# Performance work log

Hardware: AMD Instinct MI355X
Metric: run time of the kernel (lower is better)

Reference implementation:

```python
import jax, jax.numpy as jnp
import numpy as np

N = 50000       # nodes
E = 800000      # edges (before self-loops)
NFEAT = 256
NHID = 64
NHEADS = 4
NOUT = 256
NEG_SLOPE = 0.2
BN_EPS = 1e-5
LN_EPS = 1e-5


def setup_inputs() -> dict:
    key = jax.random.key(0)
    ks = jax.random.split(key, 12)
    g = lambda k, s: (jax.random.normal(k, s, dtype=jnp.float32) * 0.05)
    inp = {
        "x": jax.random.normal(ks[0], (N, NFEAT), dtype=jnp.float32),
        "edge_index": jax.random.randint(ks[1], (2, E), 0, N, dtype=jnp.int32),
        # layer 1: GATConv(NFEAT, NHID, heads=NHEADS, concat=True)
        "W1": g(ks[2], (NFEAT, NHEADS * NHID)),
        "att_src1": g(ks[3], (NHEADS, NHID)),
        "att_dst1": g(ks[4], (NHEADS, NHID)),
        "bias1": jnp.zeros((NHEADS * NHID,), jnp.float32),
        # layer 2: GATConv(NHEADS*NHID, NOUT, heads=1, concat=False)
        "W2": g(ks[5], (NHEADS * NHID, NOUT)),
        "att_src2": g(ks[6], (1, NOUT)),
        "att_dst2": g(ks[7], (1, NOUT)),
        "bias2": jnp.zeros((NOUT,), jnp.float32),
        # BatchNorm1d (eval mode: running stats)
        "bn_gamma": jnp.ones((NOUT,), jnp.float32),
        "bn_beta": jnp.zeros((NOUT,), jnp.float32),
        "bn_mean": g(ks[8], (NOUT,)),
        "bn_var": jnp.ones((NOUT,), jnp.float32),
        # LayerNorm
        "ln_gamma": jnp.ones((NOUT,), jnp.float32),
        "ln_beta": jnp.zeros((NOUT,), jnp.float32),
    }
    return inp


def _gat_conv(x, edge_index, W, att_src, att_dst, bias, concat):
    """PyG-style GATConv (eval mode, add_self_loops=True)."""
    n = x.shape[0]
    H, C = att_src.shape
    xp = (x @ W).reshape(n, H, C)                    # [N,H,C]
    loop = jnp.arange(n, dtype=edge_index.dtype)
    src = jnp.concatenate([edge_index[0], loop])     # message source j
    dst = jnp.concatenate([edge_index[1], loop])     # aggregation target i
    a_src = jnp.einsum("nhc,hc->nh", xp, att_src)    # [N,H]
    a_dst = jnp.einsum("nhc,hc->nh", xp, att_dst)
    e = jax.nn.leaky_relu(a_src[src] + a_dst[dst], NEG_SLOPE)  # [Etot,H]
    # segment softmax over edges sharing the same dst
    m = jax.ops.segment_max(e, dst, num_segments=n)
    e = jnp.exp(e - m[dst])
    denom = jax.ops.segment_sum(e, dst, num_segments=n)
    alpha = e / (denom[dst] + 1e-16)                 # [Etot,H]
    out = jax.ops.segment_sum(alpha[:, :, None] * xp[src], dst, num_segments=n)  # [N,H,C]
    out = out.reshape(n, H * C) if concat else out.mean(axis=1)
    return out + bias


def reference(x, edge_index, W1, att_src1, att_dst1, bias1,
              W2, att_src2, att_dst2, bias2,
              bn_gamma, bn_beta, bn_mean, bn_var, ln_gamma, ln_beta):
    # eval mode: F.dropout is identity
    h = jax.nn.elu(_gat_conv(x, edge_index, W1, att_src1, att_dst1, bias1, True))
    h = jax.nn.elu(_gat_conv(h, edge_index, W2, att_src2, att_dst2, bias2, False))
    # BatchNorm1d (eval: running stats)
    h = (h - bn_mean) * jax.lax.rsqrt(bn_var + BN_EPS) * bn_gamma + bn_beta
    # LayerNorm over last dim
    mu = h.mean(axis=-1, keepdims=True)
    var = jnp.mean((h - mu) ** 2, axis=-1, keepdims=True)
    h = (h - mu) * jax.lax.rsqrt(var + LN_EPS) * ln_gamma + ln_beta
    return h
```

## Files before the change

### kernel.cpp

```cpp
#include <hip/hip_runtime.h>
#include <cstddef>
#include <cstdint>

#define NNODES 50000
#define NEDGES 800000
#define FDIM   256

#define SCAN_BLOCKS 256
#define SCAN_CHUNK  ((NNODES + SCAN_BLOCKS - 1) / SCAN_BLOCKS)

typedef __attribute__((ext_vector_type(8))) short short8;
typedef __attribute__((ext_vector_type(8))) unsigned short ushort8;
typedef __attribute__((ext_vector_type(4))) float f32x4;

__device__ __forceinline__ float leaky_exp(float a) {
    float e = a > 0.f ? a : 0.2f * a;
    return __expf(e);
}
__device__ __forceinline__ unsigned short f2bf(float f) {
    uint32_t u = __builtin_bit_cast(uint32_t, f);
    u += 0x7fffu + ((u >> 16) & 1u);
    return (unsigned short)(u >> 16);
}
__device__ __forceinline__ float bf2f(unsigned short h) {
    uint32_t u = ((uint32_t)h) << 16;
    return __builtin_bit_cast(float, u);
}
__device__ __forceinline__ float bflo(uint32_t u) {
    return __builtin_bit_cast(float, u << 16);
}
__device__ __forceinline__ float bfhi(uint32_t u) {
    return __builtin_bit_cast(float, u & 0xffff0000u);
}
__device__ __forceinline__ float rlanef(float v, int l) {
    return __builtin_bit_cast(float,
        __builtin_amdgcn_readlane(__builtin_bit_cast(int, v), l));
}

__global__ __launch_bounds__(256) void cvt_k(const float* __restrict__ in,
                                             unsigned short* __restrict__ out,
                                             int n8) {
    int i = blockIdx.x * 256 + threadIdx.x;
    if (i >= n8) return;
    const float4* p = (const float4*)in + (size_t)i * 2;
    float4 a = p[0], b = p[1];
    ushort8 r;
    r[0] = f2bf(a.x); r[1] = f2bf(a.y); r[2] = f2bf(a.z); r[3] = f2bf(a.w);
    r[4] = f2bf(b.x); r[5] = f2bf(b.y); r[6] = f2bf(b.z); r[7] = f2bf(b.w);
    *(ushort8*)(out + (size_t)i * 8) = r;
}

__global__ __launch_bounds__(256) void wprep_k(const float* __restrict__ W,
                                               unsigned short* __restrict__ Wt) {
    int n = blockIdx.x, k = threadIdx.x;
    Wt[n * 256 + k] = f2bf(W[k * 256 + n]);
}

__global__ __launch_bounds__(256) void gemm_mfma(const unsigned short* __restrict__ A,
                                                 const unsigned short* __restrict__ Bt,
                                                 unsigned short* __restrict__ C, int M) {
    __shared__ unsigned short As[128 * 64];
    __shared__ unsigned short Bs[128 * 64];
    const int t = threadIdx.x;
    const int lane = t & 63, wid = t >> 6;
    const int wr = wid >> 1, wc = wid & 1;
    const int bm = blockIdx.x * 128;
    const int bn = blockIdx.y * 128;
    f32x4 acc[4][4] = {};
    const int lrow = t >> 3, lslot = t & 7;
    for (int k0 = 0; k0 < 256; k0 += 64) {
        __syncthreads();
#pragma unroll
        for (int i = 0; i < 4; ++i) {
            int row = lrow + 32 * i;
            int ga = bm + row; ga = ga < M ? ga : M - 1;
            uint4 av = *(const uint4*)(A + (size_t)ga * FDIM + k0 + lslot * 8);
            *(uint4*)(As + row * 64 + ((lslot ^ (row & 7)) << 3)) = av;
            uint4 bv = *(const uint4*)(Bt + (size_t)(bn + row) * FDIM + k0 + lslot * 8);
            *(uint4*)(Bs + row * 64 + ((lslot ^ (row & 7)) << 3)) = bv;
        }
        __syncthreads();
#pragma unroll
        for (int ks = 0; ks < 2; ++ks) {
            const int kq = ks * 4 + (lane >> 4);
            short8 a[4], b[4];
#pragma unroll
            for (int f = 0; f < 4; ++f) {
                int ra = wr * 64 + f * 16 + (lane & 15);
                a[f] = *(const short8*)(As + ra * 64 + ((kq ^ (ra & 7)) << 3));
                int rb = wc * 64 + f * 16 + (lane & 15);
                b[f] = *(const short8*)(Bs + rb * 64 + ((kq ^ (rb & 7)) << 3));
            }
#pragma unroll
            for (int mf = 0; mf < 4; ++mf)
#pragma unroll
                for (int nf = 0; nf < 4; ++nf)
                    acc[mf][nf] = __builtin_amdgcn_mfma_f32_16x16x32_bf16(
                        a[mf], b[nf], acc[mf][nf], 0, 0, 0);
        }
    }
    const int col0 = bn + wc * 64 + (lane & 15);
    const int row00 = bm + wr * 64 + (lane >> 4) * 4;
#pragma unroll
    for (int mf = 0; mf < 4; ++mf)
#pragma unroll
        for (int nf = 0; nf < 4; ++nf) {
            f32x4 v = acc[mf][nf];
            int col = col0 + nf * 16;
#pragma unroll
            for (int r = 0; r < 4; ++r) {
                int row = row00 + mf * 16 + r;
                if (row < M) C[(size_t)row * FDIM + col] = f2bf(v[r]);
            }
        }
}

template <int H>
__global__ __launch_bounds__(256) void aprep_k(const unsigned short* __restrict__ xp,
                                               const float* __restrict__ atts,
                                               const float* __restrict__ attd,
                                               float* __restrict__ as_,
                                               float* __restrict__ ad_) {
    const int lane = threadIdx.x & 63;
    const int n = blockIdx.x * 4 + (threadIdx.x >> 6);
    if (n >= NNODES) return;
    const int c = lane << 2;
    ushort4 u = *(const ushort4*)(xp + (size_t)n * FDIM + c);
    float v0 = bf2f(u.x), v1 = bf2f(u.y), v2 = bf2f(u.z), v3 = bf2f(u.w);
    float4 s4 = *(const float4*)(atts + c);
    float4 d4 = *(const float4*)(attd + c);
    float ss = v0 * s4.x + v1 * s4.y + v2 * s4.z + v3 * s4.w;
    float sd = v0 * d4.x + v1 * d4.y + v2 * d4.z + v3 * d4.w;
    constexpr int G = 64 / H;
#pragma unroll
    for (int off = 1; off < G; off <<= 1) {
        ss += __shfl_xor(ss, off);
        sd += __shfl_xor(sd, off);
    }
    if ((lane & (G - 1)) == 0) {
        int h = lane / G;
        as_[n * H + h] = ss;
        ad_[n * H + h] = sd;
    }
}

__global__ __launch_bounds__(256) void hist_k(const int* __restrict__ ei,
                                              int* __restrict__ deg) {
    int e = blockIdx.x * 256 + threadIdx.x;
    if (e < NEDGES) atomicAdd(&deg[ei[NEDGES + e]], 1);
}

__global__ __launch_bounds__(256) void scanA_k(const int* __restrict__ deg,
                                               int* __restrict__ bsum) {
    const int b = blockIdx.x, t = threadIdx.x;
    const int i = b * SCAN_CHUNK + t;
    int v = (t < SCAN_CHUNK && i < NNODES) ? deg[i] : 0;
#pragma unroll
    for (int off = 1; off < 64; off <<= 1) v += __shfl_xor(v, off);
    __shared__ int ws[4];
    if ((t & 63) == 0) ws[t >> 6] = v;
    __syncthreads();
    if (t == 0) bsum[b] = ws[0] + ws[1] + ws[2] + ws[3];
}

__global__ __launch_bounds__(256) void scanB_k(const int* __restrict__ bsum,
                                               int* __restrict__ boff,
                                               int* __restrict__ rowptr) {
    const int t = threadIdx.x;
    const int lane = t & 63, wid = t >> 6;
    int orig = bsum[t];
    int v = orig;
#pragma unroll
    for (int off = 1; off < 64; off <<= 1) {
        int u = __shfl_up(v, off);
        if (lane >= off) v += u;
    }
    __shared__ int ws[4], wo[4];
    if (lane == 63) ws[wid] = v;
    __syncthreads();
    if (t == 0) {
        int a = 0;
        for (int k = 0; k < 4; ++k) { wo[k] = a; a += ws[k]; }
        rowptr[NNODES] = a;
    }
    __syncthreads();
    boff[t] = wo[wid] + v - orig;
}

__global__ __launch_bounds__(256) void scanC_k(const int* __restrict__ deg,
                                               const int* __restrict__ boff,
                                               int* __restrict__ rowptr) {
    const int b = blockIdx.x, t = threadIdx.x;
    const int i = b * SCAN_CHUNK + t;
    const bool ok = (t < SCAN_CHUNK && i < NNODES);
    int orig = ok ? deg[i] : 0;
    int v = orig;
    const int lane = t & 63, wid = t >> 6;
#pragma unroll
    for (int off = 1; off < 64; off <<= 1) {
        int u = __shfl_up(v, off);
        if (lane >= off) v += u;
    }
    __shared__ int ws[4], wo[4];
    if (lane == 63) ws[wid] = v;
    __syncthreads();
    if (t == 0) {
        int a = 0;
        for (int k = 0; k < 4; ++k) { wo[k] = a; a += ws[k]; }
    }
    __syncthreads();
    if (ok) rowptr[i] = boff[b] + wo[wid] + v - orig;
}

__global__ __launch_bounds__(256) void scatter_k(const int* __restrict__ ei,
                                                 const int* __restrict__ rowptr,
                                                 int* __restrict__ deg,
                                                 int* __restrict__ ssrc) {
    int e = blockIdx.x * 256 + threadIdx.x;
    if (e >= NEDGES) return;
    int s = ei[e], d = ei[NEDGES + e];
    int old = atomicSub(&deg[d], 1);
    ssrc[rowptr[d + 1] - old] = s;
}

__global__ __launch_bounds__(256) void gather1_k(const unsigned short* __restrict__ xp,
                                                 const float* __restrict__ as_,
                                                 const float* __restrict__ ad_,
                                                 const int* __restrict__ rowptr,
                                                 const int* __restrict__ ssrc,
                                                 const float* __restrict__ bias,
                                                 unsigned short* __restrict__ out) {
    const int lane = threadIdx.x & 63;
    const int n = blockIdx.x * 4 + (threadIdx.x >> 6);
    if (n >= NNODES) return;
    const int h = lane >> 4;
    const int c = lane << 2;
    const int eloc = lane >> 2;
    const int hh = lane & 3;
    const float adW = ad_[n * 4 + hh];
    float a0 = 0.f, a1 = 0.f, a2 = 0.f, a3 = 0.f, den = 0.f;
    const int beg = rowptr[n], end = rowptr[n + 1];
    for (int base = beg; base < end; base += 16) {
        int my_e = base + eloc;
        float wv = 0.f; int sv = 0;
        if (my_e < end) {
            sv = ssrc[my_e];
            wv = leaky_exp(as_[sv * 4 + hh] + adW);
        }
        const int cnt = min(16, end - base);
        int e = 0;
        for (; e + 4 <= cnt; e += 4) {
            int s0 = __builtin_amdgcn_readlane(sv, (e + 0) << 2);
            int s1 = __builtin_amdgcn_readlane(sv, (e + 1) << 2);
            int s2 = __builtin_amdgcn_readlane(sv, (e + 2) << 2);
            int s3 = __builtin_amdgcn_readlane(sv, (e + 3) << 2);
            uint2 u0 = *(const uint2*)(xp + (((unsigned)s0 << 8) + (unsigned)c));
            uint2 u1 = *(const uint2*)(xp + (((unsigned)s1 << 8) + (unsigned)c));
            uint2 u2 = *(const uint2*)(xp + (((unsigned)s2 << 8) + (unsigned)c));
            uint2 u3 = *(const uint2*)(xp + (((unsigned)s3 << 8) + (unsigned)c));
            float w0 = __shfl(wv, ((e + 0) << 2) | h);
            float w1 = __shfl(wv, ((e + 1) << 2) | h);
            float w2 = __shfl(wv, ((e + 2) << 2) | h);
            float w3 = __shfl(wv, ((e + 3) << 2) | h);
            a0 += w0 * bflo(u0.x) + w1 * bflo(u1.x) + w2 * bflo(u2.x) + w3 * bflo(u3.x);
            a1 += w0 * bfhi(u0.x) + w1 * bfhi(u1.x) + w2 * bfhi(u2.x) + w3 * bfhi(u3.x);
            a2 += w0 * bflo(u0.y) + w1 * bflo(u1.y) + w2 * bflo(u2.y) + w3 * bflo(u3.y);
            a3 += w0 * bfhi(u0.y) + w1 * bfhi(u1.y) + w2 * bfhi(u2.y) + w3 * bfhi(u3.y);
            den += (w0 + w1) + (w2 + w3);
        }
        for (; e < cnt; ++e) {
            int s0 = __builtin_amdgcn_readlane(sv, e << 2);
            uint2 u0 = *(const uint2*)(xp + (((unsigned)s0 << 8) + (unsigned)c));
            float w0 = __shfl(wv, (e << 2) | h);
            a0 += w0 * bflo(u0.x); a1 += w0 * bfhi(u0.x);
            a2 += w0 * bflo(u0.y); a3 += w0 * bfhi(u0.y);
            den += w0;
        }
    }
    {
        float w = leaky_exp(as_[n * 4 + h] + ad_[n * 4 + h]);
        uint2 u = *(const uint2*)(xp + (((unsigned)n << 8) + (unsigned)c));
        a0 += w * bflo(u.x); a1 += w * bfhi(u.x);
        a2 += w * bflo(u.y); a3 += w * bfhi(u.y);
        den += w;
    }
    const float inv = 1.f / (den + 1e-16f);
    float4 b4 = *(const float4*)(bias + c);
    float o[4] = {a0 * inv + b4.x, a1 * inv + b4.y,
                  a2 * inv + b4.z, a3 * inv + b4.w};
#pragma unroll
    for (int j = 0; j < 4; ++j) o[j] = o[j] > 0.f ? o[j] : __expf(o[j]) - 1.f;
    ushort4 r;
    r.x = f2bf(o[0]); r.y = f2bf(o[1]); r.z = f2bf(o[2]); r.w = f2bf(o[3]);
    *(ushort4*)(out + (size_t)n * FDIM + c) = r;
}

__global__ __launch_bounds__(256) void gather2_k(const unsigned short* __restrict__ xp,
                                                 const float* __restrict__ as_,
                                                 const float* __restrict__ ad_,
                                                 const int* __restrict__ rowptr,
                                                 const int* __restrict__ ssrc,
                                                 const float* __restrict__ bias,
                                                 const float* __restrict__ bng,
                                                 const float* __restrict__ bnb,
                                                 const float* __restrict__ bnm,
                                                 const float* __restrict__ bnv,
                                                 const float* __restrict__ lng,
                                                 const float* __restrict__ lnb,
                                                 float* __restrict__ out) {
    const int lane = threadIdx.x & 63;
    const int n = blockIdx.x * 4 + (threadIdx.x >> 6);
    if (n >= NNODES) return;
    const int c = lane << 2;
    const float adn = ad_[n];
    float a0 = 0.f, a1 = 0.f, a2 = 0.f, a3 = 0.f, den = 0.f;
    const int beg = rowptr[n], end = rowptr[n + 1];
    for (int base = beg; base < end; base += 64) {
        int my_e = base + lane;
        float wv = 0.f; int sv = 0;
        if (my_e < end) {
            sv = ssrc[my_e];
            wv = leaky_exp(as_[sv] + adn);
        }
        const int cnt = min(64, end - base);
        int e = 0;
        for (; e + 4 <= cnt; e += 4) {
            int s0 = __builtin_amdgcn_readlane(sv, e + 0);
            int s1 = __builtin_amdgcn_readlane(sv, e + 1);
            int s2 = __builtin_amdgcn_readlane(sv, e + 2);
            int s3 = __builtin_amdgcn_readlane(sv, e + 3);
            uint2 u0 = *(const uint2*)(xp + (((unsigned)s0 << 8) + (unsigned)c));
            uint2 u1 = *(const uint2*)(xp + (((unsigned)s1 << 8) + (unsigned)c));
            uint2 u2 = *(const uint2*)(xp + (((unsigned)s2 << 8) + (unsigned)c));
            uint2 u3 = *(const uint2*)(xp + (((unsigned)s3 << 8) + (unsigned)c));
            float w0 = rlanef(wv, e + 0);
            float w1 = rlanef(wv, e + 1);
            float w2 = rlanef(wv, e + 2);
            float w3 = rlanef(wv, e + 3);
            a0 += w0 * bflo(u0.x) + w1 * bflo(u1.x) + w2 * bflo(u2.x) + w3 * bflo(u3.x);
            a1 += w0 * bfhi(u0.x) + w1 * bfhi(u1.x) + w2 * bfhi(u2.x) + w3 * bfhi(u3.x);
            a2 += w0 * bflo(u0.y) + w1 * bflo(u1.y) + w2 * bflo(u2.y) + w3 * bflo(u3.y);
            a3 += w0 * bfhi(u0.y) + w1 * bfhi(u1.y) + w2 * bfhi(u2.y) + w3 * bfhi(u3.y);
            den += (w0 + w1) + (w2 + w3);
        }
        for (; e < cnt; ++e) {
            int s0 = __builtin_amdgcn_readlane(sv, e);
            uint2 u0 = *(const uint2*)(xp + (((unsigned)s0 << 8) + (unsigned)c));
            float w0 = rlanef(wv, e);
            a0 += w0 * bflo(u0.x); a1 += w0 * bfhi(u0.x);
            a2 += w0 * bflo(u0.y); a3 += w0 * bfhi(u0.y);
            den += w0;
        }
    }
    {
        float w = leaky_exp(as_[n] + adn);
        uint2 u = *(const uint2*)(xp + (((unsigned)n << 8) + (unsigned)c));
        a0 += w * bflo(u.x); a1 += w * bfhi(u.x);
        a2 += w * bflo(u.y); a3 += w * bfhi(u.y);
        den += w;
    }
    const float inv = 1.f / (den + 1e-16f);
    float vals[4] = {a0 * inv, a1 * inv, a2 * inv, a3 * inv};
#pragma unroll
    for (int j = 0; j < 4; ++j) {
        float o = vals[j] + bias[c + j];
        o = o > 0.f ? o : __expf(o) - 1.f;
        o = (o - bnm[c + j]) * rsqrtf(bnv[c + j] + 1e-5f) * bng[c + j]
            + bnb[c + j];
        vals[j] = o;
    }
    float s1 = vals[0] + vals[1] + vals[2] + vals[3];
    float s2 = vals[0] * vals[0] + vals[1] * vals[1] +
               vals[2] * vals[2] + vals[3] * vals[3];
#pragma unroll
    for (int off = 1; off < 64; off <<= 1) {
        s1 += __shfl_xor(s1, off);
        s2 += __shfl_xor(s2, off);
    }
    float mu  = s1 * (1.f / 256.f);
    float var = s2 * (1.f / 256.f) - mu * mu;
    float r   = rsqrtf(var + 1e-5f);
#pragma unroll
    for (int j = 0; j < 4; ++j)
        out[(size_t)n * FDIM + c + j] = (vals[j] - mu) * r * lng[c + j] + lnb[c + j];
}

extern "C" void kernel_launch(void* const* d_in, const int* in_sizes, int n_in,
                              void* d_out, int out_size, void* d_ws, size_t ws_size,
                              hipStream_t stream) {
    const float* x      = (const float*)d_in[0];
    const int*   ei     = (const int*)d_in[1];
    const float* W1     = (const float*)d_in[2];
    const float* atts1  = (const float*)d_in[3];
    const float* attd1  = (const float*)d_in[4];
    const float* bias1  = (const float*)d_in[5];
    const float* W2     = (const float*)d_in[6];
    const float* atts2  = (const float*)d_in[7];
    const float* attd2  = (const float*)d_in[8];
    const float* bias2  = (const float*)d_in[9];
    const float* bng    = (const float*)d_in[10];
    const float* bnb    = (const float*)d_in[11];
    const float* bnm    = (const float*)d_in[12];
    const float* bnv    = (const float*)d_in[13];
    const float* lng    = (const float*)d_in[14];
    const float* lnb    = (const float*)d_in[15];

    const size_t NF = (size_t)NNODES * FDIM;
    unsigned short* xpbf = (unsigned short*)d_ws;
    unsigned short* xbf  = xpbf + NF;
    unsigned short* wt1  = xbf + NF;
    unsigned short* wt2  = wt1 + 65536;
    float* as1   = (float*)(wt2 + 65536);
    float* ad1   = as1 + (size_t)NNODES * 4;
    float* as2   = ad1 + (size_t)NNODES * 4;
    float* ad2   = as2 + NNODES;
    int*   deg    = (int*)(ad2 + NNODES);
    int*   rowptr = deg + NNODES;
    int*   bsum   = rowptr + (NNODES + 1);
    int*   boff   = bsum + SCAN_BLOCKS;
    int*   ssrc   = boff + SCAN_BLOCKS;
    float* outf  = (float*)d_out;

    const dim3 gemm_grid((NNODES + 127) / 128, 2);
    const int node_wave_blocks = (NNODES + 3) / 4;
    const int edge_thread_blocks = (NEDGES + 255) / 256;
    const int cvt_blocks = (int)((NF / 8 + 255) / 256);

    cvt_k<<<cvt_blocks, 256, 0, stream>>>(x, xbf, (int)(NF / 8));
    wprep_k<<<256, 256, 0, stream>>>(W1, wt1);
    wprep_k<<<256, 256, 0, stream>>>(W2, wt2);
    hipMemsetAsync(deg, 0, NNODES * sizeof(int), stream);
    hist_k<<<edge_thread_blocks, 256, 0, stream>>>(ei, deg);
    scanA_k<<<SCAN_BLOCKS, 256, 0, stream>>>(deg, bsum);
    scanB_k<<<1, 256, 0, stream>>>(bsum, boff, rowptr);
    scanC_k<<<SCAN_BLOCKS, 256, 0, stream>>>(deg, boff, rowptr);
    scatter_k<<<edge_thread_blocks, 256, 0, stream>>>(ei, rowptr, deg, ssrc);

    gemm_mfma<<<gemm_grid, 256, 0, stream>>>(xbf, wt1, xpbf, NNODES);
    aprep_k<4><<<node_wave_blocks, 256, 0, stream>>>(xpbf, atts1, attd1, as1, ad1);
    gather1_k<<<node_wave_blocks, 256, 0, stream>>>(xpbf, as1, ad1, rowptr, ssrc,
                                                    bias1, xbf);

    gemm_mfma<<<gemm_grid, 256, 0, stream>>>(xbf, wt2, xpbf, NNODES);
    aprep_k<1><<<node_wave_blocks, 256, 0, stream>>>(xpbf, atts2, attd2, as2, ad2);
    gather2_k<<<node_wave_blocks, 256, 0, stream>>>(xpbf, as2, ad2, rowptr, ssrc,
                                                    bias2, bng, bnb, bnm, bnv,
                                                    lng, lnb, outf);
}
```

Baseline: 284.3 us.

## Switch intermediates to fp16, unroll gathers by eight, reduce denominators via shuffles

```diff
diff --git a/kernel.cpp b/kernel.cpp
--- a/kernel.cpp
+++ b/kernel.cpp
@@ -9,7 +9,7 @@
 #define SCAN_BLOCKS 256
 #define SCAN_CHUNK  ((NNODES + SCAN_BLOCKS - 1) / SCAN_BLOCKS)
 
-typedef __attribute__((ext_vector_type(8))) short short8;
+typedef __attribute__((ext_vector_type(8))) _Float16 f16x8;
 typedef __attribute__((ext_vector_type(8))) unsigned short ushort8;
 typedef __attribute__((ext_vector_type(4))) float f32x4;
 
@@ -17,20 +17,16 @@
     float e = a > 0.f ? a : 0.2f * a;
     return __expf(e);
 }
-__device__ __forceinline__ unsigned short f2bf(float f) {
-    uint32_t u = __builtin_bit_cast(uint32_t, f);
-    u += 0x7fffu + ((u >> 16) & 1u);
-    return (unsigned short)(u >> 16);
-}
-__device__ __forceinline__ float bf2f(unsigned short h) {
-    uint32_t u = ((uint32_t)h) << 16;
-    return __builtin_bit_cast(float, u);
-}
-__device__ __forceinline__ float bflo(uint32_t u) {
-    return __builtin_bit_cast(float, u << 16);
-}
-__device__ __forceinline__ float bfhi(uint32_t u) {
-    return __builtin_bit_cast(float, u & 0xffff0000u);
+__device__ __forceinline__ unsigned short f2h(float f) {
+    return __builtin_bit_cast(unsigned short, (_Float16)f);
+}
+__device__ __forceinline__ float hlo(uint32_t u) {
+    _Float16 h = __builtin_bit_cast(_Float16, (unsigned short)(u & 0xffffu));
+    return (float)h;
+}
+__device__ __forceinline__ float hhi(uint32_t u) {
+    _Float16 h = __builtin_bit_cast(_Float16, (unsigned short)(u >> 16));
+    return (float)h;
 }
 __device__ __forceinline__ float rlanef(float v, int l) {
     return __builtin_bit_cast(float,
@@ -45,15 +41,15 @@
     const float4* p = (const float4*)in + (size_t)i * 2;
     float4 a = p[0], b = p[1];
     ushort8 r;
-    r[0] = f2bf(a.x); r[1] = f2bf(a.y); r[2] = f2bf(a.z); r[3] = f2bf(a.w);
-    r[4] = f2bf(b.x); r[5] = f2bf(b.y); r[6] = f2bf(b.z); r[7] = f2bf(b.w);
+    r[0] = f2h(a.x); r[1] = f2h(a.y); r[2] = f2h(a.z); r[3] = f2h(a.w);
+    r[4] = f2h(b.x); r[5] = f2h(b.y); r[6] = f2h(b.z); r[7] = f2h(b.w);
     *(ushort8*)(out + (size_t)i * 8) = r;
 }
 
 __global__ __launch_bounds__(256) void wprep_k(const float* __restrict__ W,
                                                unsigned short* __restrict__ Wt) {
     int n = blockIdx.x, k = threadIdx.x;
-    Wt[n * 256 + k] = f2bf(W[k * 256 + n]);
+    Wt[n * 256 + k] = f2h(W[k * 256 + n]);
 }
 
 __global__ __launch_bounds__(256) void gemm_mfma(const unsigned short* __restrict__ A,
@@ -83,19 +79,19 @@
 #pragma unroll
         for (int ks = 0; ks < 2; ++ks) {
             const int kq = ks * 4 + (lane >> 4);
-            short8 a[4], b[4];
+            f16x8 a[4], b[4];
 #pragma unroll
             for (int f = 0; f < 4; ++f) {
                 int ra = wr * 64 + f * 16 + (lane & 15);
-                a[f] = *(const short8*)(As + ra * 64 + ((kq ^ (ra & 7)) << 3));
+                a[f] = *(const f16x8*)(As + ra * 64 + ((kq ^ (ra & 7)) << 3));
                 int rb = wc * 64 + f * 16 + (lane & 15);
-                b[f] = *(const short8*)(Bs + rb * 64 + ((kq ^ (rb & 7)) << 3));
+                b[f] = *(const f16x8*)(Bs + rb * 64 + ((kq ^ (rb & 7)) << 3));
             }
 #pragma unroll
             for (int mf = 0; mf < 4; ++mf)
 #pragma unroll
                 for (int nf = 0; nf < 4; ++nf)
-                    acc[mf][nf] = __builtin_amdgcn_mfma_f32_16x16x32_bf16(
+                    acc[mf][nf] = __builtin_amdgcn_mfma_f32_16x16x32_f16(
                         a[mf], b[nf], acc[mf][nf], 0, 0, 0);
         }
     }
@@ -110,7 +106,7 @@
 #pragma unroll
             for (int r = 0; r < 4; ++r) {
                 int row = row00 + mf * 16 + r;
-                if (row < M) C[(size_t)row * FDIM + col] = f2bf(v[r]);
+                if (row < M) C[(size_t)row * FDIM + col] = f2h(v[r]);
             }
         }
 }
@@ -125,8 +121,8 @@
     const int n = blockIdx.x * 4 + (threadIdx.x >> 6);
     if (n >= NNODES) return;
     const int c = lane << 2;
-    ushort4 u = *(const ushort4*)(xp + (size_t)n * FDIM + c);
-    float v0 = bf2f(u.x), v1 = bf2f(u.y), v2 = bf2f(u.z), v3 = bf2f(u.w);
+    uint2 u = *(const uint2*)(xp + (size_t)n * FDIM + c);
+    float v0 = hlo(u.x), v1 = hhi(u.x), v2 = hlo(u.y), v3 = hhi(u.y);
     float4 s4 = *(const float4*)(atts + c);
     float4 d4 = *(const float4*)(attd + c);
     float ss = v0 * s4.x + v1 * s4.y + v2 * s4.z + v3 * s4.w;
@@ -247,41 +243,41 @@
             sv = ssrc[my_e];
             wv = leaky_exp(as_[sv * 4 + hh] + adW);
         }
+        float dred = wv;
+#pragma unroll
+        for (int off = 4; off < 64; off <<= 1) dred += __shfl_xor(dred, off);
+        den += __shfl(dred, h);
         const int cnt = min(16, end - base);
         int e = 0;
-        for (; e + 4 <= cnt; e += 4) {
-            int s0 = __builtin_amdgcn_readlane(sv, (e + 0) << 2);
-            int s1 = __builtin_amdgcn_readlane(sv, (e + 1) << 2);
-            int s2 = __builtin_amdgcn_readlane(sv, (e + 2) << 2);
-            int s3 = __builtin_amdgcn_readlane(sv, (e + 3) << 2);
-            uint2 u0 = *(const uint2*)(xp + (((unsigned)s0 << 8) + (unsigned)c));
-            uint2 u1 = *(const uint2*)(xp + (((unsigned)s1 << 8) + (unsigned)c));
-            uint2 u2 = *(const uint2*)(xp + (((unsigned)s2 << 8) + (unsigned)c));
-            uint2 u3 = *(const uint2*)(xp + (((unsigned)s3 << 8) + (unsigned)c));
-            float w0 = __shfl(wv, ((e + 0) << 2) | h);
-            float w1 = __shfl(wv, ((e + 1) << 2) | h);
-            float w2 = __shfl(wv, ((e + 2) << 2) | h);
-            float w3 = __shfl(wv, ((e + 3) << 2) | h);
-            a0 += w0 * bflo(u0.x) + w1 * bflo(u1.x) + w2 * bflo(u2.x) + w3 * bflo(u3.x);
-            a1 += w0 * bfhi(u0.x) + w1 * bfhi(u1.x) + w2 * bfhi(u2.x) + w3 * bfhi(u3.x);
-            a2 += w0 * bflo(u0.y) + w1 * bflo(u1.y) + w2 * bflo(u2.y) + w3 * bflo(u3.y);
-            a3 += w0 * bfhi(u0.y) + w1 * bfhi(u1.y) + w2 * bfhi(u2.y) + w3 * bfhi(u3.y);
-            den += (w0 + w1) + (w2 + w3);
+        for (; e + 8 <= cnt; e += 8) {
+            uint2 u[8]; float w[8];
+#pragma unroll
+            for (int q = 0; q < 8; ++q) {
+                int sq = __builtin_amdgcn_readlane(sv, (e + q) << 2);
+                u[q] = *(const uint2*)(xp + (((unsigned)sq << 8) + (unsigned)c));
+                w[q] = __shfl(wv, ((e + q) << 2) | h);
+            }
+#pragma unroll
+            for (int q = 0; q < 8; ++q) {
+                a0 = fmaf(hlo(u[q].x), w[q], a0);
+                a1 = fmaf(hhi(u[q].x), w[q], a1);
+                a2 = fmaf(hlo(u[q].y), w[q], a2);
+                a3 = fmaf(hhi(u[q].y), w[q], a3);
+            }
         }
         for (; e < cnt; ++e) {
-            int s0 = __builtin_amdgcn_readlane(sv, e << 2);
-            uint2 u0 = *(const uint2*)(xp + (((unsigned)s0 << 8) + (unsigned)c));
+            int sq = __builtin_amdgcn_readlane(sv, e << 2);
+            uint2 u0 = *(const uint2*)(xp + (((unsigned)sq << 8) + (unsigned)c));
             float w0 = __shfl(wv, (e << 2) | h);
-            a0 += w0 * bflo(u0.x); a1 += w0 * bfhi(u0.x);
-            a2 += w0 * bflo(u0.y); a3 += w0 * bfhi(u0.y);
-            den += w0;
+            a0 = fmaf(hlo(u0.x), w0, a0); a1 = fmaf(hhi(u0.x), w0, a1);
+            a2 = fmaf(hlo(u0.y), w0, a2); a3 = fmaf(hhi(u0.y), w0, a3);
         }
     }
     {
         float w = leaky_exp(as_[n * 4 + h] + ad_[n * 4 + h]);
         uint2 u = *(const uint2*)(xp + (((unsigned)n << 8) + (unsigned)c));
-        a0 += w * bflo(u.x); a1 += w * bfhi(u.x);
-        a2 += w * bflo(u.y); a3 += w * bfhi(u.y);
+        a0 = fmaf(hlo(u.x), w, a0); a1 = fmaf(hhi(u.x), w, a1);
+        a2 = fmaf(hlo(u.y), w, a2); a3 = fmaf(hhi(u.y), w, a3);
         den += w;
     }
     const float inv = 1.f / (den + 1e-16f);
@@ -291,7 +287,7 @@
 #pragma unroll
     for (int j = 0; j < 4; ++j) o[j] = o[j] > 0.f ? o[j] : __expf(o[j]) - 1.f;
     ushort4 r;
-    r.x = f2bf(o[0]); r.y = f2bf(o[1]); r.z = f2bf(o[2]); r.w = f2bf(o[3]);
+    r.x = f2h(o[0]); r.y = f2h(o[1]); r.z = f2h(o[2]); r.w = f2h(o[3]);
     *(ushort4*)(out + (size_t)n * FDIM + c) = r;
 }
 
@@ -322,41 +318,41 @@
             sv = ssrc[my_e];
             wv = leaky_exp(as_[sv] + adn);
         }
+        float dred = wv;
+#pragma unroll
+        for (int off = 1; off < 64; off <<= 1) dred += __shfl_xor(dred, off);
+        den += dred;
         const int cnt = min(64, end - base);
         int e = 0;
-        for (; e + 4 <= cnt; e += 4) {
-            int s0 = __builtin_amdgcn_readlane(sv, e + 0);
-            int s1 = __builtin_amdgcn_readlane(sv, e + 1);
-            int s2 = __builtin_amdgcn_readlane(sv, e + 2);
-            int s3 = __builtin_amdgcn_readlane(sv, e + 3);
-            uint2 u0 = *(const uint2*)(xp + (((unsigned)s0 << 8) + (unsigned)c));
-            uint2 u1 = *(const uint2*)(xp + (((unsigned)s1 << 8) + (unsigned)c));
-            uint2 u2 = *(const uint2*)(xp + (((unsigned)s2 << 8) + (unsigned)c));
-            uint2 u3 = *(const uint2*)(xp + (((unsigned)s3 << 8) + (unsigned)c));
-            float w0 = rlanef(wv, e + 0);
-            float w1 = rlanef(wv, e + 1);
-            float w2 = rlanef(wv, e + 2);
-            float w3 = rlanef(wv, e + 3);
-            a0 += w0 * bflo(u0.x) + w1 * bflo(u1.x) + w2 * bflo(u2.x) + w3 * bflo(u3.x);
-            a1 += w0 * bfhi(u0.x) + w1 * bfhi(u1.x) + w2 * bfhi(u2.x) + w3 * bfhi(u3.x);
-            a2 += w0 * bflo(u0.y) + w1 * bflo(u1.y) + w2 * bflo(u2.y) + w3 * bflo(u3.y);
-            a3 += w0 * bfhi(u0.y) + w1 * bfhi(u1.y) + w2 * bfhi(u2.y) + w3 * bfhi(u3.y);
-            den += (w0 + w1) + (w2 + w3);
+        for (; e + 8 <= cnt; e += 8) {
+            uint2 u[8]; float w[8];
+#pragma unroll
+            for (int q = 0; q < 8; ++q) {
+                int sq = __builtin_amdgcn_readlane(sv, e + q);
+                u[q] = *(const uint2*)(xp + (((unsigned)sq << 8) + (unsigned)c));
+                w[q] = rlanef(wv, e + q);
+            }
+#pragma unroll
+            for (int q = 0; q < 8; ++q) {
+                a0 = fmaf(hlo(u[q].x), w[q], a0);
+                a1 = fmaf(hhi(u[q].x), w[q], a1);
+                a2 = fmaf(hlo(u[q].y), w[q], a2);
+                a3 = fmaf(hhi(u[q].y), w[q], a3);
+            }
         }
         for (; e < cnt; ++e) {
-            int s0 = __builtin_amdgcn_readlane(sv, e);
-            uint2 u0 = *(const uint2*)(xp + (((unsigned)s0 << 8) + (unsigned)c));
+            int sq = __builtin_amdgcn_readlane(sv, e);
+            uint2 u0 = *(const uint2*)(xp + (((unsigned)sq << 8) + (unsigned)c));
             float w0 = rlanef(wv, e);
-            a0 += w0 * bflo(u0.x); a1 += w0 * bfhi(u0.x);
-            a2 += w0 * bflo(u0.y); a3 += w0 * bfhi(u0.y);
-            den += w0;
+            a0 = fmaf(hlo(u0.x), w0, a0); a1 = fmaf(hhi(u0.x), w0, a1);
+            a2 = fmaf(hlo(u0.y), w0, a2); a3 = fmaf(hhi(u0.y), w0, a3);
         }
     }
     {
         float w = leaky_exp(as_[n] + adn);
         uint2 u = *(const uint2*)(xp + (((unsigned)n << 8) + (unsigned)c));
-        a0 += w * bflo(u.x); a1 += w * bfhi(u.x);
-        a2 += w * bflo(u.y); a3 += w * bfhi(u.y);
+        a0 = fmaf(hlo(u.x), w, a0); a1 = fmaf(hhi(u.x), w, a1);
+        a2 = fmaf(hlo(u.y), w, a2); a3 = fmaf(hhi(u.y), w, a3);
         den += w;
     }
     const float inv = 1.f / (den + 1e-16f);
```

Result: no change. 286.5 us (+0.8%).
